# Performance work log

Hardware: AMD Instinct MI355X
Metric: run time of the kernel (lower is better)

Reference implementation:

```python
import jax, jax.numpy as jnp
import numpy as np

VOCAB = 28996
EMBED = 512
N = 8192


def setup_inputs() -> dict:
    key = jax.random.key(0)
    k1, k2, k3, k4 = jax.random.split(key, 4)
    x = jax.random.normal(k1, (N, EMBED), dtype=jnp.float32)
    y = jax.random.randint(k2, (N,), 0, VOCAB, dtype=jnp.int64 if jax.config.jax_enable_x64 else jnp.int32)
    # nn.Linear params: weight (vocab, embed), bias (vocab,)
    W = jax.random.normal(k3, (VOCAB, EMBED), dtype=jnp.float32) * 0.02
    b = jax.random.normal(k4, (VOCAB,), dtype=jnp.float32) * 0.02
    return {"x": x, "y": y, "W": W, "b": b}


def reference(x, y, W, b):
    # Decoder: linear -> softmax over vocab (dim=1)
    logits = jnp.einsum("ne,ve->nv", x, W) + b          # (N, VOCAB)
    probs = jax.nn.softmax(logits, axis=1)              # first softmax (faithful to original)
    # nn.CrossEntropyLoss applied to probs: mean over nodes of
    #   logsumexp(probs) - probs[y]   (i.e., -log_softmax(probs)[y])
    logp = jax.nn.log_softmax(probs, axis=1)            # second (redundant) softmax pass
    nll = -jnp.take_along_axis(logp, y[:, None].astype(jnp.int32), axis=1)[:, 0]
    return jnp.mean(nll)
```

## Files before the change

kernel.cpp:

```cpp
#include <hip/hip_runtime.h>
#include <stdint.h>

#define VOCAB 28996
#define EMBED 512
#define NROWS 8192
#define VPAD  29056
#define LOG2E 1.4426950408889634f
#define WSCALE 16.0f
#define INV_WSCALE_L2E (LOG2E / 16.0f)

typedef __attribute__((ext_vector_type(4)))  int   i32x4;
typedef __attribute__((ext_vector_type(8)))  int   i32x8;
typedef __attribute__((ext_vector_type(16))) float f32x16;

__device__ __forceinline__ void gload_lds16(const void* g, void* l) {
  __builtin_amdgcn_global_load_lds(
      (__attribute__((address_space(1))) const void*)g,
      (__attribute__((address_space(3))) void*)l, 16, 0, 0);
}

__device__ __forceinline__ int pk_fp8x4(float a, float b, float c, float d) {
  int r = __builtin_amdgcn_cvt_pk_fp8_f32(a, b, 0, false);
  r = __builtin_amdgcn_cvt_pk_fp8_f32(c, d, r, true);
  return r;
}

__device__ __forceinline__ int pk_fp8x4v(float4 v, float s) {
  return pk_fp8x4(v.x * s, v.y * s, v.z * s, v.w * s);
}

__global__ void __launch_bounds__(256)
prep_kernel(const float* __restrict__ x, const float* __restrict__ W,
            const float* __restrict__ b, const int* __restrict__ y,
            int* __restrict__ xb, int* __restrict__ wb,
            float* __restrict__ py, float* __restrict__ sg) {
  const int bid = blockIdx.x;
  if (bid < 2048) {
    const int row  = (bid * 256 + threadIdx.x) >> 6;
    const int lane = threadIdx.x & 63;
    const int yr = y[row];
    const float4* xr = (const float4*)(x + (size_t)row * EMBED);
    const float4* wr = (const float4*)(W + (size_t)yr * EMBED);
    float d = 0.f;
#pragma unroll
    for (int t = 0; t < 2; ++t) {
      float4 a = xr[lane * 2 + t], c = wr[lane * 2 + t];
      d += a.x * c.x + a.y * c.y + a.z * c.z + a.w * c.w;
    }
#pragma unroll
    for (int m = 1; m < 64; m <<= 1) d += __shfl_xor(d, m);
    if (lane == 0) py[row] = __expf(d + b[yr]);
  } else if (bid < 5680) {
    int i = ((bid - 2048) * 256 + threadIdx.x) * 16;
    const int VK = VOCAB * EMBED;
    int4 o;
    if (i < VK) {
      const float4* p = (const float4*)(W + i);
      o.x = pk_fp8x4v(p[0], WSCALE);
      o.y = pk_fp8x4v(p[1], WSCALE);
      o.z = pk_fp8x4v(p[2], WSCALE);
      o.w = pk_fp8x4v(p[3], WSCALE);
    } else { o.x = 0; o.y = 0; o.z = 0; o.w = 0; }
    *(int4*)(wb + i / 4) = o;
  } else if (bid < 6704) {
    int i = ((bid - 5680) * 256 + threadIdx.x) * 16;
    const float4* p = (const float4*)(x + i);
    int4 o;
    o.x = pk_fp8x4v(p[0], 1.f);
    o.y = pk_fp8x4v(p[1], 1.f);
    o.z = pk_fp8x4v(p[2], 1.f);
    o.w = pk_fp8x4v(p[3], 1.f);
    *(int4*)(xb + i / 4) = o;
  } else {
    int i = (bid - 6704) * 256 + threadIdx.x;
    sg[i] = 0.f;
  }
}

__global__ void __launch_bounds__(256, 4)
gemm_stats_kernel(const uint8_t* __restrict__ xb, const uint8_t* __restrict__ wb,
                  const float* __restrict__ bias, float* __restrict__ sg) {
  __shared__ uint8_t lA[128 * 128];
  __shared__ uint8_t lB[128 * 128];

  const int tid  = threadIdx.x;
  const int lane = tid & 63;
  const int w    = tid >> 6;
  const int l31  = lane & 31;
  const int h    = lane >> 5;
  const int kx   = lane & 7;
  const int wr   = (w >> 1) * 64;
  const int wc   = (w & 1) * 64;
  const int rowBase = blockIdx.x * 128;
  const int colBase = blockIdx.y * 128;

  f32x16 acc[2][2];
#pragma unroll
  for (int i = 0; i < 2; ++i)
#pragma unroll
    for (int j = 0; j < 2; ++j)
#pragma unroll
      for (int r = 0; r < 16; ++r) acc[i][j][r] = 0.f;

  const int srow = lane >> 3;
  const int skel = ((lane & 7) ^ srow) * 16;

  const int aBase = (wr + l31) * 128;
  const int bBase = (wc + l31) * 128;

  for (int kt = 0; kt < 4; ++kt) {
    const int k0 = kt * 128;
#pragma unroll
    for (int t = 0; t < 4; ++t) {
      const int c = w * 4 + t;
      const int r = c * 8 + srow;
      gload_lds16(xb + (size_t)(rowBase + r) * EMBED + k0 + skel, &lA[c * 1024]);
      gload_lds16(wb + (size_t)(colBase + r) * EMBED + k0 + skel, &lB[c * 1024]);
    }
    __syncthreads();
#pragma unroll
    for (int kk = 0; kk < 2; ++kk) {
      const int c0 = ((kk * 4 + h * 2) ^ kx) << 4;
      const int c1 = c0 ^ 16;
      i32x8 bq[2];
#pragma unroll
      for (int jj = 0; jj < 2; ++jj) {
        const int base = bBase + jj * 32 * 128;
        i32x4 lo = *(const i32x4*)&lB[base + c0];
        i32x4 hi = *(const i32x4*)&lB[base + c1];
        bq[jj] = __builtin_shufflevector(lo, hi, 0, 1, 2, 3, 4, 5, 6, 7);
      }
#pragma unroll
      for (int ii = 0; ii < 2; ++ii) {
        const int base = aBase + ii * 32 * 128;
        i32x4 lo = *(const i32x4*)&lA[base + c0];
        i32x4 hi = *(const i32x4*)&lA[base + c1];
        i32x8 af = __builtin_shufflevector(lo, hi, 0, 1, 2, 3, 4, 5, 6, 7);
        acc[ii][0] = __builtin_amdgcn_mfma_scale_f32_32x32x64_f8f6f4(
            af, bq[0], acc[ii][0], 0, 0, 0, 0x7F7F7F7F, 0, 0x7F7F7F7F);
        acc[ii][1] = __builtin_amdgcn_mfma_scale_f32_32x32x64_f8f6f4(
            af, bq[1], acc[ii][1], 0, 0, 0, 0x7F7F7F7F, 0, 0x7F7F7F7F);
      }
    }
    __syncthreads();
  }

  float bvl[2];
#pragma unroll
  for (int jj = 0; jj < 2; ++jj) {
    const int col = colBase + wc + jj * 32 + l31;
    bvl[jj] = (col < VOCAB) ? bias[col] * LOG2E : -1e30f;
  }

  float sp[32];
#pragma unroll
  for (int ii = 0; ii < 2; ++ii)
#pragma unroll
    for (int r = 0; r < 16; ++r)
      sp[ii * 16 + r] = exp2f(fmaf(acc[ii][0][r], INV_WSCALE_L2E, bvl[0])) +
                        exp2f(fmaf(acc[ii][1][r], INV_WSCALE_L2E, bvl[1]));

  float t1[16];
#pragma unroll
  for (int u = 0; u < 16; ++u) {
    float a = sp[2 * u]     + __shfl_xor(sp[2 * u],     1);
    float b = sp[2 * u + 1] + __shfl_xor(sp[2 * u + 1], 1);
    t1[u] = (l31 & 1) ? b : a;
  }
  float t2[8];
#pragma unroll
  for (int u = 0; u < 8; ++u) {
    float a = t1[2 * u]     + __shfl_xor(t1[2 * u],     2);
    float b = t1[2 * u + 1] + __shfl_xor(t1[2 * u + 1], 2);
    t2[u] = (l31 & 2) ? b : a;
  }
  float t3[4];
#pragma unroll
  for (int u = 0; u < 4; ++u) {
    float a = t2[2 * u]     + __shfl_xor(t2[2 * u],     4);
    float b = t2[2 * u + 1] + __shfl_xor(t2[2 * u + 1], 4);
    t3[u] = (l31 & 4) ? b : a;
  }
  float t4[2];
#pragma unroll
  for (int u = 0; u < 2; ++u) {
    float a = t3[2 * u]     + __shfl_xor(t3[2 * u],     8);
    float b = t3[2 * u + 1] + __shfl_xor(t3[2 * u + 1], 8);
    t4[u] = (l31 & 8) ? b : a;
  }
  {
    float a = t4[0] + __shfl_xor(t4[0], 16);
    float b = t4[1] + __shfl_xor(t4[1], 16);
    float ssum = (l31 & 16) ? b : a;
    const int v = l31;
    const int row = rowBase + wr + (v >> 4) * 32 + (v & 3) + 8 * ((v & 15) >> 2) + 4 * h;
    atomicAdd(&sg[row], ssum);
  }
}

__global__ void __launch_bounds__(1024)
finalize_kernel(const float* __restrict__ sg, const float* __restrict__ py,
                float* __restrict__ out) {
  __shared__ float red[1024];
  float a = 0.f;
  for (int i = threadIdx.x; i < NROWS; i += 1024)
    a += py[i] / sg[i];
  red[threadIdx.x] = a;
  __syncthreads();
  for (int st = 512; st > 0; st >>= 1) {
    if (threadIdx.x < st) red[threadIdx.x] += red[threadIdx.x + st];
    __syncthreads();
  }
  if (threadIdx.x == 0)
    out[0] = logf((float)(VOCAB + 1)) - red[0] * (1.f / (float)NROWS);
}

extern "C" void kernel_launch(void* const* d_in, const int* in_sizes, int n_in,
                              void* d_out, int out_size, void* d_ws, size_t ws_size,
                              hipStream_t stream) {
  const float* x = (const float*)d_in[0];
  const int*   y = (const int*)d_in[1];
  const float* W = (const float*)d_in[2];
  const float* b = (const float*)d_in[3];

  char* ws = (char*)d_ws;
  uint8_t* xb = (uint8_t*)ws;
  uint8_t* wb = (uint8_t*)(ws + 4194304);
  float*   sg = (float*)(ws + 4194304 + 14876672);
  float*   py = sg + NROWS;

  prep_kernel<<<6736, 256, 0, stream>>>(x, W, b, y, (int*)xb, (int*)wb, py, sg);
  gemm_stats_kernel<<<dim3(64, 227), 256, 0, stream>>>(xb, wb, b, sg);
  finalize_kernel<<<1, 1024, 0, stream>>>(sg, py, (float*)d_out);
}
```

Measured before the change: 280.3 us.

## Store fp8 operands in MFMA fragment layout and load directly from global

The prep kernel now writes the fp8-converted x and W into a fragment-major layout, so each lane's 32-byte MFMA operand is contiguous. The GEMM kernel drops the LDS staging and barriers and loads operands straight from global memory into registers, with the k loop fully unrolled. This removes the LDS round trip and sync cost, but each wave now fetches its own tiles without sharing them through LDS, which raises global/L2 traffic. The occupancy hint drops from 4 to 3 to make room for the extra registers.

```diff
diff --git a/kernel.cpp b/kernel.cpp
--- a/kernel.cpp
+++ b/kernel.cpp
@@ -9,15 +9,8 @@
 #define WSCALE 16.0f
 #define INV_WSCALE_L2E (LOG2E / 16.0f)
 
-typedef __attribute__((ext_vector_type(4)))  int   i32x4;
 typedef __attribute__((ext_vector_type(8)))  int   i32x8;
 typedef __attribute__((ext_vector_type(16))) float f32x16;
-
-__device__ __forceinline__ void gload_lds16(const void* g, void* l) {
-  __builtin_amdgcn_global_load_lds(
-      (__attribute__((address_space(1))) const void*)g,
-      (__attribute__((address_space(3))) void*)l, 16, 0, 0);
-}
 
 __device__ __forceinline__ int pk_fp8x4(float a, float b, float c, float d) {
   int r = __builtin_amdgcn_cvt_pk_fp8_f32(a, b, 0, false);
@@ -27,6 +20,11 @@
 
 __device__ __forceinline__ int pk_fp8x4v(float4 v, float s) {
   return pk_fp8x4(v.x * s, v.y * s, v.z * s, v.w * s);
+}
+
+__device__ __forceinline__ size_t frag_addr(int r, int k) {
+  return ((size_t)((r >> 5) * 8 + (k >> 6)) << 11) +
+         ((((k >> 5) & 1) * 32 + (r & 31)) << 5) + (k & 31);
 }
 
 __global__ void __launch_bounds__(256)
@@ -53,6 +51,7 @@
   } else if (bid < 5680) {
     int i = ((bid - 2048) * 256 + threadIdx.x) * 16;
     const int VK = VOCAB * EMBED;
+    const int r = i >> 9, k = i & 511;
     int4 o;
     if (i < VK) {
       const float4* p = (const float4*)(W + i);
@@ -61,39 +60,41 @@
       o.z = pk_fp8x4v(p[2], WSCALE);
       o.w = pk_fp8x4v(p[3], WSCALE);
     } else { o.x = 0; o.y = 0; o.z = 0; o.w = 0; }
-    *(int4*)(wb + i / 4) = o;
+    *(int4*)((uint8_t*)wb + frag_addr(r, k)) = o;
   } else if (bid < 6704) {
     int i = ((bid - 5680) * 256 + threadIdx.x) * 16;
+    const int r = i >> 9, k = i & 511;
     const float4* p = (const float4*)(x + i);
     int4 o;
     o.x = pk_fp8x4v(p[0], 1.f);
     o.y = pk_fp8x4v(p[1], 1.f);
     o.z = pk_fp8x4v(p[2], 1.f);
     o.w = pk_fp8x4v(p[3], 1.f);
-    *(int4*)(xb + i / 4) = o;
+    *(int4*)((uint8_t*)xb + frag_addr(r, k)) = o;
   } else {
     int i = (bid - 6704) * 256 + threadIdx.x;
     sg[i] = 0.f;
   }
 }
 
-__global__ void __launch_bounds__(256, 4)
+__global__ void __launch_bounds__(256, 3)
 gemm_stats_kernel(const uint8_t* __restrict__ xb, const uint8_t* __restrict__ wb,
                   const float* __restrict__ bias, float* __restrict__ sg) {
-  __shared__ uint8_t lA[128 * 128];
-  __shared__ uint8_t lB[128 * 128];
-
   const int tid  = threadIdx.x;
   const int lane = tid & 63;
   const int w    = tid >> 6;
   const int l31  = lane & 31;
   const int h    = lane >> 5;
-  const int kx   = lane & 7;
   const int wr   = (w >> 1) * 64;
   const int wc   = (w & 1) * 64;
   const int rowBase = blockIdx.x * 128;
   const int colBase = blockIdx.y * 128;
 
+  const int rbB = blockIdx.x * 4 + (w >> 1) * 2;
+  const int cbB = blockIdx.y * 4 + (w & 1) * 2;
+  const uint8_t* pa = xb + ((size_t)rbB << 14) + lane * 32;
+  const uint8_t* pb = wb + ((size_t)cbB << 14) + lane * 32;
+
   f32x16 acc[2][2];
 #pragma unroll
   for (int i = 0; i < 2; ++i)
@@ -102,47 +103,28 @@
 #pragma unroll
       for (int r = 0; r < 16; ++r) acc[i][j][r] = 0.f;
 
-  const int srow = lane >> 3;
-  const int skel = ((lane & 7) ^ srow) * 16;
-
-  const int aBase = (wr + l31) * 128;
-  const int bBase = (wc + l31) * 128;
-
+#pragma unroll
   for (int kt = 0; kt < 4; ++kt) {
-    const int k0 = kt * 128;
-#pragma unroll
-    for (int t = 0; t < 4; ++t) {
-      const int c = w * 4 + t;
-      const int r = c * 8 + srow;
-      gload_lds16(xb + (size_t)(rowBase + r) * EMBED + k0 + skel, &lA[c * 1024]);
-      gload_lds16(wb + (size_t)(colBase + r) * EMBED + k0 + skel, &lB[c * 1024]);
+    i32x8 bq[2][2], aq[2][2];
+#pragma unroll
+    for (int kk = 0; kk < 2; ++kk) {
+      const size_t off = (size_t)(kt * 2 + kk) << 11;
+#pragma unroll
+      for (int jj = 0; jj < 2; ++jj)
+        bq[kk][jj] = *(const i32x8*)(pb + ((size_t)jj << 14) + off);
+#pragma unroll
+      for (int ii = 0; ii < 2; ++ii)
+        aq[kk][ii] = *(const i32x8*)(pa + ((size_t)ii << 14) + off);
     }
-    __syncthreads();
-#pragma unroll
-    for (int kk = 0; kk < 2; ++kk) {
-      const int c0 = ((kk * 4 + h * 2) ^ kx) << 4;
-      const int c1 = c0 ^ 16;
-      i32x8 bq[2];
-#pragma unroll
-      for (int jj = 0; jj < 2; ++jj) {
-        const int base = bBase + jj * 32 * 128;
-        i32x4 lo = *(const i32x4*)&lB[base + c0];
-        i32x4 hi = *(const i32x4*)&lB[base + c1];
-        bq[jj] = __builtin_shufflevector(lo, hi, 0, 1, 2, 3, 4, 5, 6, 7);
+#pragma unroll
+    for (int kk = 0; kk < 2; ++kk)
+#pragma unroll
+      for (int ii = 0; ii < 2; ++ii) {
+        acc[ii][0] = __builtin_amdgcn_mfma_scale_f32_32x32x64_f8f6f4(
+            aq[kk][ii], bq[kk][0], acc[ii][0], 0, 0, 0, 0x7F7F7F7F, 0, 0x7F7F7F7F);
+        acc[ii][1] = __builtin_amdgcn_mfma_scale_f32_32x32x64_f8f6f4(
+            aq[kk][ii], bq[kk][1], acc[ii][1], 0, 0, 0, 0x7F7F7F7F, 0, 0x7F7F7F7F);
       }
-#pragma unroll
-      for (int ii = 0; ii < 2; ++ii) {
-        const int base = aBase + ii * 32 * 128;
-        i32x4 lo = *(const i32x4*)&lA[base + c0];
-        i32x4 hi = *(const i32x4*)&lA[base + c1];
-        i32x8 af = __builtin_shufflevector(lo, hi, 0, 1, 2, 3, 4, 5, 6, 7);
-        acc[ii][0] = __builtin_amdgcn_mfma_scale_f32_32x32x64_f8f6f4(
-            af, bq[0], acc[ii][0], 0, 0, 0, 0x7F7F7F7F, 0, 0x7F7F7F7F);
-        acc[ii][1] = __builtin_amdgcn_mfma_scale_f32_32x32x64_f8f6f4(
-            af, bq[1], acc[ii][1], 0, 0, 0, 0x7F7F7F7F, 0, 0x7F7F7F7F);
-      }
-    }
-    __syncthreads();
   }
 
   float bvl[2];
```

Measured after the change: 267.4 us. 1.05x faster.
